# Kernel tuning notes

Measured on AMD Instinct MI355X. Metric: run time of the kernel, lower is better.

The kernel has to match this reference:

```python
import jax, jax.numpy as jnp
import numpy as np

NUM_HEADS = 16


def setup_inputs() -> dict:
    key = jax.random.key(0)
    k1, k2, k3 = jax.random.split(key, 3)
    b, d, s = 2, 1024, 2048
    x = jax.random.normal(k1, (b, d, s), dtype=jnp.float32)
    # torch nn.Linear(d, 3d) without bias == x @ W1 with W1 of shape (d, 3d)
    W1 = jax.random.normal(k2, (d, 3 * d), dtype=jnp.float32) * (d ** -0.5)
    W2 = jax.random.normal(k3, (d, d), dtype=jnp.float32) * (d ** -0.5)
    return {"x": x, "W1": W1, "W2": W2}


def reference(x, W1, W2):
    # x: (b, hidden_dim, s) -> (b, s, hidden_dim)
    b, d, s = x.shape
    h = NUM_HEADS
    hd = d // h
    xt = jnp.swapaxes(x, 1, 2)                       # (b, s, d)
    qkv = xt @ W1                                    # (b, s, 3d)
    qkv = qkv.reshape(b, s, 3, h, hd)
    qkv = jnp.transpose(qkv, (2, 0, 3, 1, 4))        # (3, b, h, s, hd)
    q, k, v = qkv[0], qkv[1], qkv[2]
    scale = hd ** -0.5
    scores = jnp.einsum("bhqd,bhkd->bhqk", q, k) * scale  # (b, h, s, s)
    # causal mask: same as torch code (adds float32 min where not lower-tri)
    neg = jnp.finfo(jnp.float32).min
    causal = jnp.tril(jnp.ones((s, s), dtype=bool))
    scores = jnp.where(causal[None, None, :, :], scores, scores + neg)
    attn = jax.nn.softmax(scores, axis=-1)           # dropout = identity (eval)
    out = jnp.einsum("bhqk,bhkd->bhqd", attn, v)     # (b, h, s, hd)
    out = jnp.transpose(out, (0, 2, 1, 3)).reshape(b, s, d)
    out = out @ W2                                   # (b, s, d)
    return jnp.swapaxes(out, 1, 2)                   # (b, d, s)
```

## Files before the change

kernel.cpp:

```cpp
#include <hip/hip_runtime.h>
#include <math.h>

#define B_  2
#define D_  1024
#define S_  2048
#define H_  16
#define HD_ 64
#define D3_ 3072
#define M_  4096

typedef __attribute__((ext_vector_type(8))) short short8;
typedef __attribute__((ext_vector_type(4))) float float4v;

__device__ __forceinline__ short f2bf(float f) {
    unsigned u = __builtin_bit_cast(unsigned, f);
    unsigned r = (u + 0x7FFFu + ((u >> 16) & 1u)) >> 16;
    return (short)r;
}

__device__ __forceinline__ unsigned cvt_pk_bf16(float lo, float hi) {
    unsigned r;
    asm("v_cvt_pk_bf16_f32 %0, %1, %2" : "=v"(r) : "v"(lo), "v"(hi));
    return r;
}

__device__ __forceinline__ float fast_exp2(float x) {
    float r;
    asm("v_exp_f32 %0, %1" : "=v"(r) : "v"(x));
    return r;
}

#define GLD16(gsrc, ldst)                                                      \
    __builtin_amdgcn_global_load_lds(                                          \
        (const __attribute__((address_space(1))) void*)(gsrc),                 \
        (__attribute__((address_space(3))) void*)(ldst), 16, 0, 0)

__global__ __launch_bounds__(256) void transpose_cvt_all(const float* __restrict__ x,
                                                         short* __restrict__ xt,
                                                         const float* __restrict__ W1,
                                                         short* __restrict__ W1t,
                                                         const float* __restrict__ W2,
                                                         short* __restrict__ W2t) {
    __shared__ short t[64][66];
    const int bid = (int)blockIdx.x;
    const float* in;
    short* out;
    int C, R, rb, cb;
    if (bid < 1024) {
        const int z = bid >> 9, tt = bid & 511;
        R = D_; C = S_;
        cb = tt & 31; rb = tt >> 5;
        in = x + (size_t)z * D_ * S_;
        out = xt + (size_t)z * D_ * S_;
    } else if (bid < 1792) {
        const int tt = bid - 1024;
        R = D_; C = D3_;
        cb = tt % 48; rb = tt / 48;
        in = W1; out = W1t;
    } else {
        const int tt = bid - 1792;
        R = D_; C = D_;
        cb = tt & 15; rb = tt >> 4;
        in = W2; out = W2t;
    }
    const int r0 = rb * 64, c0 = cb * 64;
    const int tx = threadIdx.x & 31, ty = threadIdx.x >> 5;
    #pragma unroll
    for (int i = ty; i < 64; i += 8) {
        const float2 v = *(const float2*)&in[(size_t)(r0 + i) * C + c0 + tx * 2];
        t[i][tx * 2]     = f2bf(v.x);
        t[i][tx * 2 + 1] = f2bf(v.y);
    }
    __syncthreads();
    #pragma unroll
    for (int j = ty; j < 64; j += 8) {
        short2 v;
        v.x = t[tx * 2][j];
        v.y = t[tx * 2 + 1][j];
        *(short2*)&out[(size_t)(c0 + j) * R + r0 + tx * 2] = v;
    }
}

__device__ __forceinline__ void gemm_core8(const short* __restrict__ A,
                                           const short* __restrict__ Bt,
                                           int m0, int n0,
                                           short* As, short* Bs,
                                           float4v acc[2][4]) {
    const int tid = threadIdx.x;
    const int lane = tid & 63, w = tid >> 6;
    const int wr = (w >> 1) * 32, wc = (w & 1) * 64;
    const int srow = lane >> 2;
    const int scol = ((lane & 3) ^ ((srow >> 1) & 3)) * 8;
    const int rr = lane & 15;
    const int kc = ((lane >> 4) ^ ((rr >> 1) & 3)) * 8;
    for (int k0 = 0; k0 < 1024; k0 += 32) {
        GLD16(A  + (size_t)(m0 + w * 16 + srow) * 1024 + k0 + scol,
              As + w * 512 + lane * 8);
        GLD16(Bt + (size_t)(n0 + w * 16 + srow) * 1024 + k0 + scol,
              Bs + w * 512 + lane * 8);
        __syncthreads();
        short8 a[2], b[4];
        #pragma unroll
        for (int m = 0; m < 2; ++m)
            a[m] = *(const short8*)&As[(wr + m * 16 + rr) * 32 + kc];
        #pragma unroll
        for (int n = 0; n < 4; ++n)
            b[n] = *(const short8*)&Bs[(wc + n * 16 + rr) * 32 + kc];
        #pragma unroll
        for (int m = 0; m < 2; ++m)
            #pragma unroll
            for (int n = 0; n < 4; ++n)
                acc[m][n] = __builtin_amdgcn_mfma_f32_16x16x32_bf16(a[m], b[n], acc[m][n], 0, 0, 0);
        __syncthreads();
    }
}

__global__ __launch_bounds__(512) void gemm_qkv_mfma(const short* __restrict__ xt,
                                                     const short* __restrict__ W1t,
                                                     short* __restrict__ q,
                                                     short* __restrict__ kk,
                                                     short* __restrict__ vt) {
    __shared__ short As[128 * 32], Bs[128 * 32];
    float4v acc[2][4];
    #pragma unroll
    for (int m = 0; m < 2; ++m)
        #pragma unroll
        for (int n = 0; n < 4; ++n) acc[m][n] = (float4v){0.f, 0.f, 0.f, 0.f};
    const int bid = (int)blockIdx.x;
    const int xcd = bid & 7, r = bid >> 3;
    const int mt = (xcd & 3) * 8 + (r & 7);
    const int nt = (xcd >> 2) * 12 + (r >> 3);
    const int m0 = mt * 128, n0 = nt * 128;
    gemm_core8(xt, W1t, m0, n0, As, Bs, acc);
    const int lane = threadIdx.x & 63, w = threadIdx.x >> 6;
    const int wr = (w >> 1) * 32, wc = (w & 1) * 64;
    const float qscale = 0.125f * 1.44269504f;
    #pragma unroll
    for (int n = 0; n < 4; ++n) {
        const int gcol = n0 + wc + n * 16 + (lane & 15);
        const int which = gcol >> 10, hh = (gcol >> 6) & 15, hd = gcol & 63;
        #pragma unroll
        for (int m = 0; m < 2; ++m) {
            #pragma unroll
            for (int ri = 0; ri < 4; ++ri) {
                const int grow = m0 + wr + m * 16 + (lane >> 4) * 4 + ri;
                const int bb = grow >> 11, ss = grow & (S_ - 1);
                float av = acc[m][n][ri];
                if (which == 0) av *= qscale;
                const short v = f2bf(av);
                if (which == 0)      q [((size_t)(bb * H_ + hh) * S_ + ss) * HD_ + hd] = v;
                else if (which == 1) kk[((size_t)(bb * H_ + hh) * S_ + ss) * HD_ + hd] = v;
                else                 vt[((size_t)(bb * H_ + hh) * HD_ + hd) * S_ + ss] = v;
            }
        }
    }
}

__global__ __launch_bounds__(256) void attn_mfma(const short* __restrict__ q,
                                                 const short* __restrict__ k,
                                                 const short* __restrict__ vt,
                                                 short* __restrict__ ao) {
    __shared__ short Ks[2][64 * 64];
    __shared__ short Vts[2][64 * 64];
    __shared__ short Ps[64 * 64];
    __shared__ float sums[64];
    const int tid = threadIdx.x;
    const int lane = tid & 63, w = tid >> 6;
    const int bid = (int)blockIdx.x;
    const int xcd = bid & 7, slot = bid >> 3;
    const int bh = xcd * 4 + (slot & 3);
    const int qpair = slot >> 2;
    const size_t base = (size_t)bh * S_ * HD_;
    const short* qp = q + base;
    const short* kp = k + base;
    const short* vp = vt + base;
    const int bb = bh >> 4, hh = bh & 15;
    const int wrow = w * 16;

    for (int half = 0; half < 2; ++half) {
        const int qt = (half == 0) ? qpair : 31 - qpair;
        const int q0 = qt * 64;
        short8 qf[2];
        #pragma unroll
        for (int ks = 0; ks < 2; ++ks)
            qf[ks] = *(const short8*)&qp[(size_t)(q0 + wrow + (lane & 15)) * HD_
                                         + ks * 32 + (lane >> 4) * 8];
        float4v accO[4];
        float lsum = 0.f;
        #pragma unroll
        for (int n = 0; n < 4; ++n) accO[n] = (float4v){0.f, 0.f, 0.f, 0.f};

        const int nkb = qt + 1;
        __syncthreads();
        #pragma unroll
        for (int j = 0; j < 2; ++j) {
            const int g = (w * 2 + j) * 64 + lane;
            const int r = g >> 3, cs = g & 7;
            const int co = (cs ^ (r & 7)) << 3;
            GLD16(kp + (size_t)r * HD_ + co, &Ks[0][g * 8]);
            GLD16(vp + (size_t)r * S_ + co,  &Vts[0][g * 8]);
        }
        int cur = 0;
        for (int kb = 0; kb < nkb; ++kb) {
            const int kv0 = kb * 64;
            __syncthreads();
            if (kb + 1 < nkb) {
                const int kv1 = kv0 + 64;
                #pragma unroll
                for (int j = 0; j < 2; ++j) {
                    const int g = (w * 2 + j) * 64 + lane;
                    const int r = g >> 3, cs = g & 7;
                    const int co = (cs ^ (r & 7)) << 3;
                    GLD16(kp + (size_t)(kv1 + r) * HD_ + co, &Ks[cur ^ 1][g * 8]);
                    GLD16(vp + (size_t)r * S_ + kv1 + co,    &Vts[cur ^ 1][g * 8]);
                }
            }
            float4v accS[4];
            #pragma unroll
            for (int n = 0; n < 4; ++n) accS[n] = (float4v){0.f, 0.f, 0.f, 0.f};
            __builtin_amdgcn_s_setprio(1);
            #pragma unroll
            for (int ks = 0; ks < 2; ++ks) {
                #pragma unroll
                for (int n = 0; n < 4; ++n) {
                    const int rowk = n * 16 + (lane & 15);
                    const int ch = ks * 4 + (lane >> 4);
                    const short8 kf = *(const short8*)&Ks[cur][rowk * 64 + ((ch ^ (rowk & 7)) << 3)];
                    accS[n] = __builtin_amdgcn_mfma_f32_16x16x32_bf16(kf, qf[ks], accS[n], 0, 0, 0);
                }
            }
            __builtin_amdgcn_s_setprio(0);
            const bool diag = (kb == qt);
            const int qg = q0 + wrow + (lane & 15);
            const int prow = wrow + (lane & 15);
            #pragma unroll
            for (int n = 0; n < 4; ++n) {
                const int kvb = kv0 + n * 16 + ((lane >> 4) << 2);
                float p[4];
                if (diag) {
                    const int dlim = qg - kvb;
                    #pragma unroll
                    for (int ri = 0; ri < 4; ++ri)
                        p[ri] = (ri <= dlim) ? fast_exp2(accS[n][ri]) : 0.f;
                } else {
                    #pragma unroll
                    for (int ri = 0; ri < 4; ++ri)
                        p[ri] = fast_exp2(accS[n][ri]);
                }
                lsum += (p[0] + p[1]) + (p[2] + p[3]);
                const unsigned lo = cvt_pk_bf16(p[0], p[1]);
                const unsigned hi = cvt_pk_bf16(p[2], p[3]);
                const int col = n * 16 + ((lane >> 4) << 2);
                const int ch = col >> 3;
                const int addr = prow * 64 + ((ch ^ (prow & 7)) << 3) + (col & 7);
                *(uint2*)&Ps[addr] = (uint2){lo, hi};
            }
            __builtin_amdgcn_s_setprio(1);
            #pragma unroll
            for (int ks = 0; ks < 2; ++ks) {
                const int prow2 = wrow + (lane & 15);
                const int chp = ks * 4 + (lane >> 4);
                const short8 pf = *(const short8*)&Ps[prow2 * 64 + ((chp ^ (prow2 & 7)) << 3)];
                #pragma unroll
                for (int n = 0; n < 4; ++n) {
                    const int vrow = n * 16 + (lane & 15);
                    const int ch = ks * 4 + (lane >> 4);
                    const short8 vf = *(const short8*)&Vts[cur][vrow * 64 + ((ch ^ (vrow & 7)) << 3)];
                    accO[n] = __builtin_amdgcn_mfma_f32_16x16x32_bf16(pf, vf, accO[n], 0, 0, 0);
                }
            }
            __builtin_amdgcn_s_setprio(0);
            cur ^= 1;
        }
        {
            float t = lsum;
            t += __shfl_xor(t, 16);
            t += __shfl_xor(t, 32);
            if (lane < 16) sums[wrow + lane] = t;
        }
        #pragma unroll
        for (int ri = 0; ri < 4; ++ri) {
            const int lrow = wrow + ((lane >> 4) << 2) + ri;
            const float inv = 1.f / sums[lrow];
            const int grow = q0 + lrow;
            #pragma unroll
            for (int n = 0; n < 4; ++n) {
                const int col = hh * 64 + n * 16 + (lane & 15);
                ao[((size_t)(bb * S_ + grow)) * D_ + col] = f2bf(accO[n][ri] * inv);
            }
        }
    }
}

__global__ __launch_bounds__(512) void gemm_out_mfma(const short* __restrict__ W2t,
                                                     const short* __restrict__ ao,
                                                     float* __restrict__ out) {
    __shared__ short As[128 * 32], Bs[128 * 32];
    float4v acc[2][4];
    #pragma unroll
    for (int m = 0; m < 2; ++m)
        #pragma unroll
        for (int n = 0; n < 4; ++n) acc[m][n] = (float4v){0.f, 0.f, 0.f, 0.f};
    const int bid = (int)blockIdx.x;
    const int xcd = bid & 7, r = bid >> 3;
    const int mt = (xcd & 1) * 4 + (r & 3);
    const int nt = (xcd >> 1) * 8 + (r >> 2);
    const int m0 = mt * 128, n0 = nt * 128;
    gemm_core8(W2t, ao, m0, n0, As, Bs, acc);
    const int lane = threadIdx.x & 63, w = threadIdx.x >> 6;
    const int wr = (w >> 1) * 32, wc = (w & 1) * 64;
    #pragma unroll
    for (int m = 0; m < 2; ++m) {
        #pragma unroll
        for (int ri = 0; ri < 4; ++ri) {
            const int grow = m0 + wr + m * 16 + (lane >> 4) * 4 + ri;
            #pragma unroll
            for (int n = 0; n < 4; ++n) {
                const int gcol = n0 + wc + n * 16 + (lane & 15);
                const int bb = gcol >> 11, ss = gcol & (S_ - 1);
                out[(size_t)bb * D_ * S_ + (size_t)grow * S_ + ss] = acc[m][n][ri];
            }
        }
    }
}

extern "C" void kernel_launch(void* const* d_in, const int* in_sizes, int n_in,
                              void* d_out, int out_size, void* d_ws, size_t ws_size,
                              hipStream_t stream) {
    const float* x  = (const float*)d_in[0];
    const float* W1 = (const float*)d_in[1];
    const float* W2 = (const float*)d_in[2];
    float* out = (float*)d_out;

    short* xt  = (short*)d_ws;
    short* W1t = xt  + (size_t)M_ * D_;
    short* W2t = W1t + (size_t)D3_ * D_;
    short* q   = W2t + (size_t)D_ * D_;
    short* kk  = q   + (size_t)B_ * H_ * S_ * HD_;
    short* vt  = kk  + (size_t)B_ * H_ * S_ * HD_;
    short* ao  = vt  + (size_t)B_ * H_ * S_ * HD_;

    transpose_cvt_all<<<dim3(2048), 256, 0, stream>>>(x, xt, W1, W1t, W2, W2t);
    gemm_qkv_mfma<<<dim3(768), 512, 0, stream>>>(xt, W1t, q, kk, vt);
    attn_mfma<<<dim3(512), 256, 0, stream>>>(q, kk, vt, ao);
    gemm_out_mfma<<<dim3(256), 512, 0, stream>>>(W2t, ao, out);
}
```

Measured before the change: 111.7 us.

## Rewrite QKV GEMM with 256x256 tiles and double-buffered LDS prefetch

```diff
diff --git a/kernel.cpp b/kernel.cpp
--- a/kernel.cpp
+++ b/kernel.cpp
@@ -81,6 +81,113 @@
     }
 }
 
+__device__ __forceinline__ void stage_half(const short* __restrict__ mat, int rowbase,
+                                           int kt, short* lds, int tid) {
+    #pragma unroll
+    for (int j = 0; j < 2; ++j) {
+        const int g = j * 512 + tid;
+        const int r = g >> 3, c = g & 7;
+        GLD16(mat + (size_t)(rowbase + r) * 1024 + kt * 64 + ((c ^ (r & 7)) << 3),
+              lds + g * 8);
+    }
+}
+
+__global__ __launch_bounds__(512, 2) void gemm_qkv_mfma(const short* __restrict__ xt,
+                                                        const short* __restrict__ W1t,
+                                                        short* __restrict__ q,
+                                                        short* __restrict__ kk,
+                                                        short* __restrict__ vt) {
+    __shared__ short As[2][16384], Bs[2][16384];
+    const int tid = threadIdx.x;
+    const int lane = tid & 63, w = tid >> 6;
+    const int wm = w >> 2, wn = w & 3;
+    const int rr = lane & 15, hi4 = lane >> 4;
+    const int swz = rr & 7;
+    const int bid = (int)blockIdx.x;
+    const int m0 = (bid & 15) * 256, n0 = (bid >> 4) * 256;
+    float4v acc[8][4];
+    #pragma unroll
+    for (int mf = 0; mf < 8; ++mf)
+        #pragma unroll
+        for (int nf = 0; nf < 4; ++nf) acc[mf][nf] = (float4v){0.f, 0.f, 0.f, 0.f};
+
+    stage_half(xt,  m0,       0, &As[0][0],    tid);
+    stage_half(xt,  m0 + 128, 0, &As[0][8192], tid);
+    stage_half(W1t, n0,       0, &Bs[0][0],    tid);
+    stage_half(W1t, n0 + 128, 0, &Bs[0][8192], tid);
+    stage_half(W1t, n0,       1, &Bs[1][0],    tid);
+    stage_half(W1t, n0 + 128, 1, &Bs[1][8192], tid);
+    asm volatile("s_waitcnt vmcnt(4)" ::: "memory");
+    asm volatile("s_barrier" ::: "memory");
+
+    for (int t = 0; t < 16; ++t) {
+        const int db = t & 1, dbn = db ^ 1;
+        short8 bf[4][2];
+        #pragma unroll
+        for (int qq = 0; qq < 4; ++qq) {
+            short8 af[2][2];
+            if (qq == 0) {
+                #pragma unroll
+                for (int nf = 0; nf < 4; ++nf)
+                    #pragma unroll
+                    for (int ks = 0; ks < 2; ++ks) {
+                        const int row = wn * 64 + nf * 16 + rr;
+                        const int ch = ks * 4 + hi4;
+                        bf[nf][ks] = *(const short8*)&Bs[db][row * 64 + ((ch ^ swz) << 3)];
+                    }
+            }
+            #pragma unroll
+            for (int mf2 = 0; mf2 < 2; ++mf2)
+                #pragma unroll
+                for (int ks = 0; ks < 2; ++ks) {
+                    const int row = wm * 128 + (qq * 2 + mf2) * 16 + rr;
+                    const int ch = ks * 4 + hi4;
+                    af[mf2][ks] = *(const short8*)&As[db][row * 64 + ((ch ^ swz) << 3)];
+                }
+            if (qq == 0 && t + 1 < 16) stage_half(xt,  m0,       t + 1, &As[dbn][0],    tid);
+            if (qq == 1 && t + 1 < 16) stage_half(xt,  m0 + 128, t + 1, &As[dbn][8192], tid);
+            if (qq == 2 && t + 2 < 16) stage_half(W1t, n0,       t + 2, &Bs[db][0],     tid);
+            if (qq == 3 && t + 2 < 16) stage_half(W1t, n0 + 128, t + 2, &Bs[db][8192],  tid);
+            asm volatile("s_waitcnt lgkmcnt(0)" ::: "memory");
+            if (qq == 3) {
+                if (t < 14) asm volatile("s_waitcnt vmcnt(4)" ::: "memory");
+                else        asm volatile("s_waitcnt vmcnt(0)" ::: "memory");
+            }
+            asm volatile("s_barrier" ::: "memory");
+            __builtin_amdgcn_s_setprio(1);
+            #pragma unroll
+            for (int ks = 0; ks < 2; ++ks)
+                #pragma unroll
+                for (int nf = 0; nf < 4; ++nf)
+                    #pragma unroll
+                    for (int mf2 = 0; mf2 < 2; ++mf2)
+                        acc[qq * 2 + mf2][nf] = __builtin_amdgcn_mfma_f32_16x16x32_bf16(
+                            af[mf2][ks], bf[nf][ks], acc[qq * 2 + mf2][nf], 0, 0, 0);
+            __builtin_amdgcn_s_setprio(0);
+        }
+    }
+    const float qscale = 0.125f * 1.44269504f;
+    #pragma unroll
+    for (int nf = 0; nf < 4; ++nf) {
+        const int gcol = n0 + wn * 64 + nf * 16 + rr;
+        const int which = gcol >> 10, hh = (gcol >> 6) & 15, hd = gcol & 63;
+        #pragma unroll
+        for (int mf = 0; mf < 8; ++mf) {
+            #pragma unroll
+            for (int ri = 0; ri < 4; ++ri) {
+                const int grow = m0 + wm * 128 + mf * 16 + hi4 * 4 + ri;
+                const int bb = grow >> 11, ss = grow & (S_ - 1);
+                float av = acc[mf][nf][ri];
+                if (which == 0) av *= qscale;
+                const short v = f2bf(av);
+                if (which == 0)      q [((size_t)(bb * H_ + hh) * S_ + ss) * HD_ + hd] = v;
+                else if (which == 1) kk[((size_t)(bb * H_ + hh) * S_ + ss) * HD_ + hd] = v;
+                else                 vt[((size_t)(bb * H_ + hh) * HD_ + hd) * S_ + ss] = v;
+            }
+        }
+    }
+}
+
 __device__ __forceinline__ void gemm_core8(const short* __restrict__ A,
                                            const short* __restrict__ Bt,
                                            int m0, int n0,
@@ -112,47 +219,6 @@
             for (int n = 0; n < 4; ++n)
                 acc[m][n] = __builtin_amdgcn_mfma_f32_16x16x32_bf16(a[m], b[n], acc[m][n], 0, 0, 0);
         __syncthreads();
-    }
-}
-
-__global__ __launch_bounds__(512) void gemm_qkv_mfma(const short* __restrict__ xt,
-                                                     const short* __restrict__ W1t,
-                                                     short* __restrict__ q,
-                                                     short* __restrict__ kk,
-                                                     short* __restrict__ vt) {
-    __shared__ short As[128 * 32], Bs[128 * 32];
-    float4v acc[2][4];
-    #pragma unroll
-    for (int m = 0; m < 2; ++m)
-        #pragma unroll
-        for (int n = 0; n < 4; ++n) acc[m][n] = (float4v){0.f, 0.f, 0.f, 0.f};
-    const int bid = (int)blockIdx.x;
-    const int xcd = bid & 7, r = bid >> 3;
-    const int mt = (xcd & 3) * 8 + (r & 7);
-    const int nt = (xcd >> 2) * 12 + (r >> 3);
-    const int m0 = mt * 128, n0 = nt * 128;
-    gemm_core8(xt, W1t, m0, n0, As, Bs, acc);
-    const int lane = threadIdx.x & 63, w = threadIdx.x >> 6;
-    const int wr = (w >> 1) * 32, wc = (w & 1) * 64;
-    const float qscale = 0.125f * 1.44269504f;
-    #pragma unroll
-    for (int n = 0; n < 4; ++n) {
-        const int gcol = n0 + wc + n * 16 + (lane & 15);
-        const int which = gcol >> 10, hh = (gcol >> 6) & 15, hd = gcol & 63;
-        #pragma unroll
-        for (int m = 0; m < 2; ++m) {
-            #pragma unroll
-            for (int ri = 0; ri < 4; ++ri) {
-                const int grow = m0 + wr + m * 16 + (lane >> 4) * 4 + ri;
-                const int bb = grow >> 11, ss = grow & (S_ - 1);
-                float av = acc[m][n][ri];
-                if (which == 0) av *= qscale;
-                const short v = f2bf(av);
-                if (which == 0)      q [((size_t)(bb * H_ + hh) * S_ + ss) * HD_ + hd] = v;
-                else if (which == 1) kk[((size_t)(bb * H_ + hh) * S_ + ss) * HD_ + hd] = v;
-                else                 vt[((size_t)(bb * H_ + hh) * HD_ + hd) * S_ + ss] = v;
-            }
-        }
     }
 }
 
@@ -341,7 +407,7 @@
     short* ao  = vt  + (size_t)B_ * H_ * S_ * HD_;
 
     transpose_cvt_all<<<dim3(2048), 256, 0, stream>>>(x, xt, W1, W1t, W2, W2t);
-    gemm_qkv_mfma<<<dim3(768), 512, 0, stream>>>(xt, W1t, q, kk, vt);
+    gemm_qkv_mfma<<<dim3(192), 512, 0, stream>>>(xt, W1t, q, kk, vt);
     attn_mfma<<<dim3(512), 256, 0, stream>>>(q, kk, vt, ao);
     gemm_out_mfma<<<dim3(256), 512, 0, stream>>>(W2t, ao, out);
 }
```

New measurement: 133.8 us. 1.2x slower.
